# Kernel tuning notes

Hardware: AMD Instinct MI355X
Metric: run time of the kernel (lower is better)

The kernel has to match this reference:

```python
import jax, jax.numpy as jnp
import numpy as np

HID = 1024
H = 8        # num_attention_heads
KV = 2       # num_key_value_heads
HD = HID // H  # head_dim = 128
G = H // KV    # kv groups = 4
EPS = 1e-6


def setup_inputs() -> dict:
    key = jax.random.key(0)
    ks = jax.random.split(key, 12)
    B, S = 4, 2048
    s = 0.02
    inp = {
        "hidden_states": jax.random.normal(ks[0], (B, S, HID), jnp.float32),
        "rope": jax.random.normal(ks[1], (1, 1, S, 2 * HD), jnp.float32),
        # q_proj outputs 2*H*HD (query + elementwise gate)
        "Wq": jax.random.normal(ks[2], (HID, 2 * H * HD), jnp.float32) * s,
        "bq": jnp.zeros((2 * H * HD,), jnp.float32),
        "Wk": jax.random.normal(ks[3], (HID, KV * HD), jnp.float32) * s,
        "bk": jnp.zeros((KV * HD,), jnp.float32),
        "Wv": jax.random.normal(ks[4], (HID, KV * HD), jnp.float32) * s,
        "bv": jnp.zeros((KV * HD,), jnp.float32),
        "Wo": jax.random.normal(ks[5], (H * HD, HID), jnp.float32) * s,
        "bo": jnp.zeros((HID,), jnp.float32),
        "q_norm_w": jnp.ones((HD,), jnp.float32),
        "k_norm_w": jnp.ones((HD,), jnp.float32),
    }
    return inp


def _rmsnorm(x, w):
    var = jnp.mean(jnp.square(x), axis=-1, keepdims=True)
    return x * jax.lax.rsqrt(var + EPS) * w


def _rot(x):
    # interleaved rotation: [-x1, x0, -x3, x2, ...]
    x2 = x.reshape(x.shape[:-1] + (HD // 2, 2))
    r = jnp.stack([-x2[..., 1], x2[..., 0]], axis=-1)
    return r.reshape(x.shape)


def _apply_rope_cat(x, emb):
    # emb: [S, 2*HD] = cat(sin, cos); x: [B, h, S, HD]
    sin, cos = jnp.split(emb, 2, axis=-1)
    sin = sin[None, None]
    cos = cos[None, None]
    return x * cos + _rot(x) * sin


def reference(hidden_states, rope, Wq, bq, Wk, bk, Wv, bv, Wo, bo, q_norm_w, k_norm_w):
    B, S, _ = hidden_states.shape
    qg = hidden_states @ Wq + bq                     # [B,S,2*H*HD]
    qg = qg.reshape(B, S, KV, -1)                    # [B,S,KV, 2*G*HD]
    q, gate = jnp.split(qg, [HD * G], axis=-1)       # [B,S,KV,G*HD], [B,S,KV,G*HD]
    gate = gate.reshape(B, S, H, HD)                 # [B,S,H,HD]
    q = q.reshape(B, S, H, HD).transpose(0, 2, 1, 3) # [B,H,S,HD]
    k = (hidden_states @ Wk + bk).reshape(B, S, KV, HD).transpose(0, 2, 1, 3)
    v = (hidden_states @ Wv + bv).reshape(B, S, KV, HD).transpose(0, 2, 1, 3)

    q = _rmsnorm(q, q_norm_w)
    k = _rmsnorm(k, k_norm_w)

    emb = rope[0, 0, :S]                             # [S, 2*HD]
    q = _apply_rope_cat(q, emb)
    k = _apply_rope_cat(k, emb)

    # GQA: repeat kv heads to match query heads
    k = jnp.repeat(k, G, axis=1)                     # [B,H,S,HD]
    v = jnp.repeat(v, G, axis=1)

    scale = 1.0 / jnp.sqrt(jnp.asarray(HD, q.dtype))
    scores = jnp.einsum("bhqd,bhkd->bhqk", q, k) * scale
    attn = jax.nn.softmax(scores, axis=-1)
    out = jnp.einsum("bhqk,bhkd->bhqd", attn, v)     # [B,H,S,HD]

    out = out.transpose(0, 2, 1, 3)                  # [B,S,H,HD]
    out = out * jax.nn.sigmoid(gate)
    out = out.reshape(B, S, H * HD)
    return out @ Wo + bo
```

## Files before the change

### kernel.cpp

```cpp
#include <hip/hip_runtime.h>
#include <math.h>

#define SCALE_ 0.08838834764831845f
#define PSHIFT 8.0f
#define LOG2E_ 1.4426950408889634f
#define PSH2_  11.541560327111707f

typedef __attribute__((ext_vector_type(8))) short short8;
typedef __attribute__((ext_vector_type(4))) float floatx4;
typedef __attribute__((ext_vector_type(4))) _Float16 half4;
typedef __attribute__((ext_vector_type(8))) _Float16 half8;

__device__ inline short f2bf(float x) {
    union { float f; unsigned u; } v; v.f = x;
    unsigned r = v.u + 0x7fff + ((v.u >> 16) & 1);
    return (short)(r >> 16);
}
__device__ inline float bf2f(short h) {
    union { float f; unsigned u; } v; v.u = ((unsigned)(unsigned short)h) << 16;
    return v.f;
}

__global__ __launch_bounds__(256) void prep_fused(
    const float* __restrict__ X, short* __restrict__ Xb,
    const float* __restrict__ bq, const float* __restrict__ bk2,
    const float* __restrict__ bv2, float* __restrict__ bcat,
    const float* __restrict__ Wq, const float* __restrict__ Wk,
    const float* __restrict__ Wv, const float* __restrict__ Wo,
    short* __restrict__ Wt, short* __restrict__ Wot)
{
    __shared__ float T[32][33];
    const int bid = blockIdx.x;
    const int t = threadIdx.x;
    if (bid < 8192) {
        const int gid = bid * 256 + t;
        if (gid < 2097152) {
            const float4 v = ((const float4*)X)[gid];
            short4 o;
            o.x = f2bf(v.x); o.y = f2bf(v.y); o.z = f2bf(v.z); o.w = f2bf(v.w);
            ((short4*)Xb)[gid] = o;
        }
        if (gid < 2560)
            bcat[gid] = (gid < 2048) ? bq[gid]
                      : (gid < 2304) ? bk2[gid - 2048] : bv2[gid - 2304];
        return;
    }
    const int t2 = bid - 8192;
    const int k0 = (t2 & 31) * 32;
    const int ny = t2 >> 5;
    const float* src; int ldn, ncol0, nrow0; short* dst;
    if (ny < 80) {
        const int n0 = ny * 32;
        if (n0 < 2048)      { src = Wq; ldn = 2048; ncol0 = n0; }
        else if (n0 < 2304) { src = Wk; ldn = 256;  ncol0 = n0 - 2048; }
        else                { src = Wv; ldn = 256;  ncol0 = n0 - 2304; }
        dst = Wt; nrow0 = n0;
    } else {
        const int n0 = (ny - 80) * 32;
        src = Wo; ldn = 1024; ncol0 = n0; dst = Wot; nrow0 = n0;
    }
    {
        const int r = t >> 3, c4 = (t & 7) * 4;
        const float4 v = *(const float4*)&src[(size_t)(k0 + r) * ldn + ncol0 + c4];
        T[r][c4 + 0] = v.x; T[r][c4 + 1] = v.y; T[r][c4 + 2] = v.z; T[r][c4 + 3] = v.w;
    }
    __syncthreads();
    {
        const int nr = t >> 3, kc4 = (t & 7) * 4;
        short4 o;
        o.x = f2bf(T[kc4 + 0][nr]);
        o.y = f2bf(T[kc4 + 1][nr]);
        o.z = f2bf(T[kc4 + 2][nr]);
        o.w = f2bf(T[kc4 + 3][nr]);
        *(short4*)&dst[(size_t)(nrow0 + nr) * 1024 + k0 + kc4] = o;
    }
}

__global__ __launch_bounds__(256) void qkv_mfma(
    const short* __restrict__ Ag, const short* __restrict__ Bg,
    const float* __restrict__ bcat,
    short* __restrict__ qb, short* __restrict__ kb,
    short* __restrict__ vb, short* __restrict__ gateb)
{
    __shared__ short As[128 * 64];
    __shared__ short Bs[128 * 64];
    const int tid = threadIdx.x;
    const int wave = tid >> 6, lane = tid & 63;
    const int quad = lane >> 4, l16 = lane & 15;
    const int wm = wave & 1, wn = wave >> 1;
    const int lin = blockIdx.x;
    const int xcd = lin & 7;
    const int idx = lin >> 3;
    const int rr_ = idx / 20;
    const int m0 = (xcd * 8 + rr_) * 128;
    const int n0 = (idx - rr_ * 20) * 128;

    floatx4 acc[4][4] = {};

    for (int k0 = 0; k0 < 1024; k0 += 64) {
        __syncthreads();
        #pragma unroll
        for (int c = 0; c < 4; ++c) {
            const int blk = (c * 4 + wave) * 64 + lane;
            const int row = blk >> 3, p = blk & 7;
            const int col = (p ^ (row & 7)) << 3;
            __builtin_amdgcn_global_load_lds(
                (const __attribute__((address_space(1))) unsigned int*)(Ag + (size_t)(m0 + row) * 1024 + k0 + col),
                (__attribute__((address_space(3))) unsigned int*)&As[(c * 4 + wave) * 512],
                16, 0, 0);
            __builtin_amdgcn_global_load_lds(
                (const __attribute__((address_space(1))) unsigned int*)(Bg + (size_t)(n0 + row) * 1024 + k0 + col),
                (__attribute__((address_space(3))) unsigned int*)&Bs[(c * 4 + wave) * 512],
                16, 0, 0);
        }
        __syncthreads();
        #pragma unroll
        for (int ks = 0; ks < 2; ++ks) {
            short8 af[4], bfr[4];
            #pragma unroll
            for (int mt = 0; mt < 4; ++mt) {
                const int row = wm * 64 + mt * 16 + l16;
                const int p = (ks * 4 + quad) ^ (row & 7);
                af[mt] = *(const short8*)&As[row * 64 + p * 8];
            }
            #pragma unroll
            for (int nt = 0; nt < 4; ++nt) {
                const int row = wn * 64 + nt * 16 + l16;
                const int p = (ks * 4 + quad) ^ (row & 7);
                bfr[nt] = *(const short8*)&Bs[row * 64 + p * 8];
            }
            #pragma unroll
            for (int mt = 0; mt < 4; ++mt)
                #pragma unroll
                for (int nt = 0; nt < 4; ++nt)
                    acc[mt][nt] = __builtin_amdgcn_mfma_f32_16x16x32_bf16(af[mt], bfr[nt], acc[mt][nt], 0, 0, 0);
        }
    }

    #pragma unroll
    for (int nt = 0; nt < 4; ++nt) {
        const int n = n0 + wn * 64 + nt * 16 + l16;
        const float bias = bcat[n];
        #pragma unroll
        for (int mt = 0; mt < 4; ++mt) {
            #pragma unroll
            for (int r = 0; r < 4; ++r) {
                const int m = m0 + wm * 64 + mt * 16 + quad * 4 + r;
                const int b = m >> 11, s = m & 2047;
                const short o = f2bf(acc[mt][nt][r] + bias);
                if (n < 2048) {
                    const int kv = n >> 10, rr = n & 1023;
                    if (rr < 512) {
                        const int h = kv * 4 + (rr >> 7), d = rr & 127;
                        qb[(((size_t)(b * 8 + h)) * 2048 + s) * 128 + d] = o;
                    } else {
                        const int r2 = rr - 512;
                        const int h = kv * 4 + (r2 >> 7), d = r2 & 127;
                        gateb[(size_t)m * 1024 + h * 128 + d] = o;
                    }
                } else if (n < 2304) {
                    const int c = n - 2048;
                    kb[(((size_t)(b * 2 + (c >> 7))) * 2048 + s) * 128 + (c & 127)] = o;
                } else {
                    const int c = n - 2304;
                    vb[(((size_t)(b * 2 + (c >> 7))) * 2048 + s) * 128 + (c & 127)] = o;
                }
            }
        }
    }
}

__global__ __launch_bounds__(256) void norm_vtrans(
    short* __restrict__ qb, short* __restrict__ kb,
    const float* __restrict__ rope,
    const float* __restrict__ qw, const float* __restrict__ kw,
    const short* __restrict__ vb, _Float16* __restrict__ vt)
{
    __shared__ float T[32][33];
    const int bid = blockIdx.x;
    const int t = threadIdx.x;
    if (bid < 20480) {
        const int row = bid * 4 + (t >> 6);
        short* base; const float* w; int s; float scl;
        if (row < 65536) { base = qb + (size_t)row * 128; s = row & 2047; w = qw; scl = SCALE_; }
        else { const int r2 = row - 65536; base = kb + (size_t)r2 * 128; s = r2 & 2047; w = kw; scl = 1.0f; }
        const int lane = t & 63;
        const short2 xv = *(const short2*)&base[lane * 2];
        const float x0 = bf2f(xv.x), x1 = bf2f(xv.y);
        float ssq = x0 * x0 + x1 * x1;
        #pragma unroll
        for (int off = 1; off < 64; off <<= 1) ssq += __shfl_xor(ssq, off);
        const float inv = rsqrtf(ssq * (1.0f / 128.0f) + 1e-6f);
        const float a = x0 * inv * w[lane * 2];
        const float b = x1 * inv * w[lane * 2 + 1];
        const float* er = rope + (size_t)s * 256;
        const float sin0 = er[lane * 2], sin1 = er[lane * 2 + 1];
        const float cos0 = er[128 + lane * 2], cos1 = er[128 + lane * 2 + 1];
        short2 o;
        o.x = f2bf((a * cos0 - b * sin0) * scl);
        o.y = f2bf((b * cos1 + a * sin1) * scl);
        *(short2*)&base[lane * 2] = o;
        return;
    }
    const int t2 = bid - 20480;
    const int s0 = (t2 & 63) * 32, d0 = ((t2 >> 6) & 3) * 32, bk = t2 >> 8;
    const short* src = vb + ((size_t)bk * 2048 + s0) * 128 + d0;
    {
        const int sr = t >> 3, c4 = (t & 7) * 4;
        const short4 xv = *(const short4*)&src[sr * 128 + c4];
        T[sr][c4 + 0] = bf2f(xv.x);
        T[sr][c4 + 1] = bf2f(xv.y);
        T[sr][c4 + 2] = bf2f(xv.z);
        T[sr][c4 + 3] = bf2f(xv.w);
    }
    __syncthreads();
    {
        const int dr = t >> 3, sc4 = (t & 7) * 4;
        const int cs = sc4 >> 2;
        const int nc = (cs < 4) ? (cs << 1) : (((cs - 4) << 1) | 1);
        half4 o;
        o[0] = (_Float16)T[sc4 + 0][dr];
        o[1] = (_Float16)T[sc4 + 1][dr];
        o[2] = (_Float16)T[sc4 + 2][dr];
        o[3] = (_Float16)T[sc4 + 3][dr];
        *(half4*)&vt[((size_t)bk * 128 + d0 + dr) * 2048 + s0 + nc * 4] = o;
    }
}

__global__ __launch_bounds__(256, 2) void attn_mfma(
    const short* __restrict__ qb, const short* __restrict__ kb,
    const _Float16* __restrict__ vt, const short* __restrict__ gateb,
    short* __restrict__ xo)
{
    __shared__ short    Ks[2][64 * 128];
    __shared__ _Float16 VTs[2][128 * 64];

    const int tid = threadIdx.x;
    const int wave = tid >> 6, lane = tid & 63;
    const int quad = lane >> 4, l16 = lane & 15;
    const int lin = blockIdx.x;
    const int idx = lin >> 3;
    const int bh = (lin & 7) * 4 + (idx >> 4);
    const int b = bh >> 3, h = bh & 7, kv = h >> 2;
    const int q0 = (idx & 15) * 128;

    short8 qf[4][2];
    #pragma unroll
    for (int u = 0; u < 2; ++u) {
        const short* qbase = qb + (((size_t)(b * 8 + h)) * 2048 + q0 + wave * 32 + u * 16 + l16) * 128;
        #pragma unroll
        for (int ks = 0; ks < 4; ++ks)
            qf[ks][u] = *(const short8*)&qbase[ks * 32 + quad * 8];
    }

    const short*    kbase  = kb + (size_t)(b * 2 + kv) * 2048 * 128;
    const _Float16* vtbase = vt + (size_t)(b * 2 + kv) * 128 * 2048;

    int koff[4], voff[4];
    #pragma unroll
    for (int c = 0; c < 4; ++c) {
        const int sidx = (c * 4 + wave) * 64 + lane;
        { const int r = sidx >> 4, p = sidx & 15;
          koff[c] = r * 128 + ((p ^ (r & 7)) << 3); }
        { const int r = sidx >> 3, p = sidx & 7;
          voff[c] = r * 2048 + ((p ^ (r & 7)) << 3); }
    }

    floatx4 O[8][2] = {};
    float lsum[2] = {0.0f, 0.0f};

    #pragma unroll
    for (int c = 0; c < 4; ++c) {
        __builtin_amdgcn_global_load_lds(
            (const __attribute__((address_space(1))) unsigned int*)(kbase + koff[c]),
            (__attribute__((address_space(3))) unsigned int*)&Ks[0][(c * 4 + wave) * 512],
            16, 0, 0);
        __builtin_amdgcn_global_load_lds(
            (const __attribute__((address_space(1))) unsigned int*)(vtbase + voff[c]),
            (__attribute__((address_space(3))) unsigned int*)&VTs[0][(c * 4 + wave) * 512],
            16, 0, 0);
    }

    for (int kt = 0; kt < 32; ++kt) {
        const int cur = kt & 1;
        __syncthreads();

        if (kt + 1 < 32) {
            const short*    kg = kbase  + (size_t)(kt + 1) * 8192;
            const _Float16* vg = vtbase + (kt + 1) * 64;
            #pragma unroll
            for (int c = 0; c < 4; ++c) {
                __builtin_amdgcn_global_load_lds(
                    (const __attribute__((address_space(1))) unsigned int*)(kg + koff[c]),
                    (__attribute__((address_space(3))) unsigned int*)&Ks[cur ^ 1][(c * 4 + wave) * 512],
                    16, 0, 0);
                __builtin_amdgcn_global_load_lds(
                    (const __attribute__((address_space(1))) unsigned int*)(vg + voff[c]),
                    (__attribute__((address_space(3))) unsigned int*)&VTs[cur ^ 1][(c * 4 + wave) * 512],
                    16, 0, 0);
            }
        }

        #pragma unroll
        for (int t = 0; t < 2; ++t) {
            floatx4 ST[2][2];
            __builtin_amdgcn_s_setprio(1);
            #pragma unroll
            for (int j = 0; j < 2; ++j) {
                ST[j][0] = (floatx4){0.f, 0.f, 0.f, 0.f};
                ST[j][1] = (floatx4){0.f, 0.f, 0.f, 0.f};
                const int krow = (2 * t + j) * 16 + l16;
                #pragma unroll
                for (int ks = 0; ks < 4; ++ks) {
                    const short8 af = *(const short8*)&Ks[cur][krow * 128 + (((ks * 4 + quad) ^ (l16 & 7)) << 3)];
                    ST[j][0] = __builtin_amdgcn_mfma_f32_16x16x32_bf16(af, qf[ks][0], ST[j][0], 0, 0, 0);
                    ST[j][1] = __builtin_amdgcn_mfma_f32_16x16x32_bf16(af, qf[ks][1], ST[j][1], 0, 0, 0);
                }
            }
            __builtin_amdgcn_s_setprio(0);

            half8 pf[2];
            #pragma unroll
            for (int u = 0; u < 2; ++u) {
                #pragma unroll
                for (int r = 0; r < 4; ++r) {
                    const float plo = exp2f(fmaf(ST[0][u][r], LOG2E_, -PSH2_));
                    const float phi = exp2f(fmaf(ST[1][u][r], LOG2E_, -PSH2_));
                    lsum[u] += plo + phi;
                    pf[u][r]     = (_Float16)plo;
                    pf[u][4 + r] = (_Float16)phi;
                }
            }

            __builtin_amdgcn_s_setprio(1);
            #pragma unroll
            for (int dt = 0; dt < 8; ++dt) {
                const half8 va = *(const half8*)&VTs[cur][(dt * 16 + l16) * 64 + (((4 * t + quad) ^ (l16 & 7)) << 3)];
                O[dt][0] = __builtin_amdgcn_mfma_f32_16x16x32_f16(va, pf[0], O[dt][0], 0, 0, 0);
                O[dt][1] = __builtin_amdgcn_mfma_f32_16x16x32_f16(va, pf[1], O[dt][1], 0, 0, 0);
            }
            __builtin_amdgcn_s_setprio(0);
        }
    }

    #pragma unroll
    for (int u = 0; u < 2; ++u) {
        float ps = lsum[u];
        ps += __shfl_xor(ps, 16);
        ps += __shfl_xor(ps, 32);
        const float invl = 1.0f / ps;
        const int s = q0 + wave * 32 + u * 16 + l16;
        const size_t base = ((size_t)b * 2048 + s) * 1024 + h * 128;
        #pragma unroll
        for (int dt = 0; dt < 8; ++dt) {
            const int d0 = dt * 16 + quad * 4;
            const short4 g4 = *(const short4*)&gateb[base + d0];
            short4 o4;
            o4.x = f2bf(O[dt][u][0] * invl * (1.0f / (1.0f + __expf(-bf2f(g4.x)))));
            o4.y = f2bf(O[dt][u][1] * invl * (1.0f / (1.0f + __expf(-bf2f(g4.y)))));
            o4.z = f2bf(O[dt][u][2] * invl * (1.0f / (1.0f + __expf(-bf2f(g4.z)))));
            o4.w = f2bf(O[dt][u][3] * invl * (1.0f / (1.0f + __expf(-bf2f(g4.w)))));
            *(short4*)&xo[base + d0] = o4;
        }
    }
}

__global__ __launch_bounds__(256) void out_mfma(
    const short* __restrict__ Ag, const short* __restrict__ Bg,
    const float* __restrict__ bo, float* __restrict__ Y)
{
    __shared__ short As[128 * 64];
    __shared__ short Bs[128 * 64];
    const int tid = threadIdx.x;
    const int wave = tid >> 6, lane = tid & 63;
    const int quad = lane >> 4, l16 = lane & 15;
    const int wm = wave & 1, wn = wave >> 1;
    const int lin = blockIdx.x;
    const int xcd = lin & 7;
    const int idx = lin >> 3;
    const int m0 = (xcd * 8 + (idx >> 3)) * 128;
    const int n0 = (idx & 7) * 128;

    floatx4 acc[4][4] = {};

    for (int k0 = 0; k0 < 1024; k0 += 64) {
        __syncthreads();
        #pragma unroll
        for (int c = 0; c < 4; ++c) {
            const int blk = (c * 4 + wave) * 64 + lane;
            const int row = blk >> 3, p = blk & 7;
            const int col = (p ^ (row & 7)) << 3;
            __builtin_amdgcn_global_load_lds(
                (const __attribute__((address_space(1))) unsigned int*)(Ag + (size_t)(m0 + row) * 1024 + k0 + col),
                (__attribute__((address_space(3))) unsigned int*)&As[(c * 4 + wave) * 512],
                16, 0, 0);
            __builtin_amdgcn_global_load_lds(
                (const __attribute__((address_space(1))) unsigned int*)(Bg + (size_t)(n0 + row) * 1024 + k0 + col),
                (__attribute__((address_space(3))) unsigned int*)&Bs[(c * 4 + wave) * 512],
                16, 0, 0);
        }
        __syncthreads();
        #pragma unroll
        for (int ks = 0; ks < 2; ++ks) {
            short8 af[4], bfr[4];
            #pragma unroll
            for (int mt = 0; mt < 4; ++mt) {
                const int row = wm * 64 + mt * 16 + l16;
                const int p = (ks * 4 + quad) ^ (row & 7);
                af[mt] = *(const short8*)&As[row * 64 + p * 8];
            }
            #pragma unroll
            for (int nt = 0; nt < 4; ++nt) {
                const int row = wn * 64 + nt * 16 + l16;
                const int p = (ks * 4 + quad) ^ (row & 7);
                bfr[nt] = *(const short8*)&Bs[row * 64 + p * 8];
            }
            #pragma unroll
            for (int mt = 0; mt < 4; ++mt)
                #pragma unroll
                for (int nt = 0; nt < 4; ++nt)
                    acc[mt][nt] = __builtin_amdgcn_mfma_f32_16x16x32_bf16(af[mt], bfr[nt], acc[mt][nt], 0, 0, 0);
        }
    }

    #pragma unroll
    for (int nt = 0; nt < 4; ++nt) {
        const int n = n0 + wn * 64 + nt * 16 + l16;
        const float bias = bo[n];
        #pragma unroll
        for (int mt = 0; mt < 4; ++mt) {
            #pragma unroll
            for (int r = 0; r < 4; ++r) {
                const int m = m0 + wm * 64 + mt * 16 + quad * 4 + r;
                Y[(size_t)m * 1024 + n] = acc[mt][nt][r] + bias;
            }
        }
    }
}

extern "C" void kernel_launch(void* const* d_in, const int* in_sizes, int n_in,
                              void* d_out, int out_size, void* d_ws, size_t ws_size,
                              hipStream_t stream) {
    (void)in_sizes; (void)n_in; (void)out_size; (void)ws_size;
    const float* hs   = (const float*)d_in[0];
    const float* rope = (const float*)d_in[1];
    const float* Wq   = (const float*)d_in[2];
    const float* bq   = (const float*)d_in[3];
    const float* Wk   = (const float*)d_in[4];
    const float* bk   = (const float*)d_in[5];
    const float* Wv   = (const float*)d_in[6];
    const float* bv   = (const float*)d_in[7];
    const float* Wo   = (const float*)d_in[8];
    const float* bo   = (const float*)d_in[9];
    const float* qw   = (const float*)d_in[10];
    const float* kw   = (const float*)d_in[11];
    float* out = (float*)d_out;

    short* qb    = (short*)d_ws;
    short* kbuf  = qb    + (size_t)8388608;
    short* vb    = kbuf  + (size_t)2097152;
    _Float16* vt = (_Float16*)(vb + (size_t)2097152);
    short* gateb = (short*)(vt + (size_t)2097152);
    short* xb    = gateb + (size_t)8388608;
    short* wt    = xb    + (size_t)8388608;
    short* wot   = wt    + (size_t)2621440;
    float* bcat  = (float*)(wot + (size_t)1048576);

    prep_fused<<<dim3(11776), 256, 0, stream>>>(hs, xb, bq, bk, bv, bcat,
                                                Wq, Wk, Wv, Wo, wt, wot);
    qkv_mfma<<<dim3(1280), 256, 0, stream>>>(xb, wt, bcat, qb, kbuf, vb, gateb);
    norm_vtrans<<<dim3(22528), 256, 0, stream>>>(qb, kbuf, rope, qw, kw, vb, vt);
    attn_mfma<<<dim3(512), 256, 0, stream>>>(qb, kbuf, vt, gateb, xb);
    out_mfma<<<dim3(512), 256, 0, stream>>>(xb, wot, bo, out);
}
```

Before: 308.1 us.

## Split attention KV tiles across two wave groups with LDS combine

The attention kernel moves from 256 to 512 threads per block. Two wave groups each process half of every 64-key tile for the same query rows, then the second group's partial O accumulators and row sums are written to LDS and merged by the first group before the gated store. The aim is more resident waves to hide latency and half the serial MFMA chain per wave. In exchange it adds a reduction through LDS and drops the s_setprio hints. The __launch_bounds__(512,4) request may also force very tight register limits, which risks spilling the O accumulators.

Measured after the change: 387.7 us. 1.26x slower.

```diff
diff --git a/kernel.cpp b/kernel.cpp
--- a/kernel.cpp
+++ b/kernel.cpp
@@ -227,17 +227,21 @@
     }
 }
 
-__global__ __launch_bounds__(256, 2) void attn_mfma(
+__global__ __launch_bounds__(512, 4) void attn_mfma(
     const short* __restrict__ qb, const short* __restrict__ kb,
     const _Float16* __restrict__ vt, const short* __restrict__ gateb,
     short* __restrict__ xo)
 {
-    __shared__ short    Ks[2][64 * 128];
-    __shared__ _Float16 VTs[2][128 * 64];
+    __shared__ __align__(16) char smem[67584];
+    short*    KsB  = (short*)smem;
+    _Float16* VTsB = (_Float16*)(smem + 32768);
+    floatx4*  comb = (floatx4*)smem;
+    float*    Lred = (float*)(smem + 65536);
 
     const int tid = threadIdx.x;
     const int wave = tid >> 6, lane = tid & 63;
     const int quad = lane >> 4, l16 = lane & 15;
+    const int qg = wave & 3, kh = wave >> 2;
     const int lin = blockIdx.x;
     const int idx = lin >> 3;
     const int bh = (lin & 7) * 4 + (idx >> 4);
@@ -247,7 +251,7 @@
     short8 qf[4][2];
     #pragma unroll
     for (int u = 0; u < 2; ++u) {
-        const short* qbase = qb + (((size_t)(b * 8 + h)) * 2048 + q0 + wave * 32 + u * 16 + l16) * 128;
+        const short* qbase = qb + (((size_t)(b * 8 + h)) * 2048 + q0 + qg * 32 + u * 16 + l16) * 128;
         #pragma unroll
         for (int ks = 0; ks < 4; ++ks)
             qf[ks][u] = *(const short8*)&qbase[ks * 32 + quad * 8];
@@ -256,10 +260,10 @@
     const short*    kbase  = kb + (size_t)(b * 2 + kv) * 2048 * 128;
     const _Float16* vtbase = vt + (size_t)(b * 2 + kv) * 128 * 2048;
 
-    int koff[4], voff[4];
+    int koff[2], voff[2];
     #pragma unroll
-    for (int c = 0; c < 4; ++c) {
-        const int sidx = (c * 4 + wave) * 64 + lane;
+    for (int c = 0; c < 2; ++c) {
+        const int sidx = (c * 8 + wave) * 64 + lane;
         { const int r = sidx >> 4, p = sidx & 15;
           koff[c] = r * 128 + ((p ^ (r & 7)) << 3); }
         { const int r = sidx >> 3, p = sidx & 7;
@@ -270,14 +274,14 @@
     float lsum[2] = {0.0f, 0.0f};
 
     #pragma unroll
-    for (int c = 0; c < 4; ++c) {
+    for (int c = 0; c < 2; ++c) {
         __builtin_amdgcn_global_load_lds(
             (const __attribute__((address_space(1))) unsigned int*)(kbase + koff[c]),
-            (__attribute__((address_space(3))) unsigned int*)&Ks[0][(c * 4 + wave) * 512],
+            (__attribute__((address_space(3))) unsigned int*)&KsB[(c * 8 + wave) * 512],
             16, 0, 0);
         __builtin_amdgcn_global_load_lds(
             (const __attribute__((address_space(1))) unsigned int*)(vtbase + voff[c]),
-            (__attribute__((address_space(3))) unsigned int*)&VTs[0][(c * 4 + wave) * 512],
+            (__attribute__((address_space(3))) unsigned int*)&VTsB[(c * 8 + wave) * 512],
             16, 0, 0);
     }
 
@@ -289,78 +293,85 @@
             const short*    kg = kbase  + (size_t)(kt + 1) * 8192;
             const _Float16* vg = vtbase + (kt + 1) * 64;
             #pragma unroll
-            for (int c = 0; c < 4; ++c) {
+            for (int c = 0; c < 2; ++c) {
                 __builtin_amdgcn_global_load_lds(
                     (const __attribute__((address_space(1))) unsigned int*)(kg + koff[c]),
-                    (__attribute__((address_space(3))) unsigned int*)&Ks[cur ^ 1][(c * 4 + wave) * 512],
+                    (__attribute__((address_space(3))) unsigned int*)&KsB[(cur ^ 1) * 8192 + (c * 8 + wave) * 512],
                     16, 0, 0);
                 __builtin_amdgcn_global_load_lds(
                     (const __attribute__((address_space(1))) unsigned int*)(vg + voff[c]),
-                    (__attribute__((address_space(3))) unsigned int*)&VTs[cur ^ 1][(c * 4 + wave) * 512],
+                    (__attribute__((address_space(3))) unsigned int*)&VTsB[(cur ^ 1) * 8192 + (c * 8 + wave) * 512],
                     16, 0, 0);
             }
         }
 
-        #pragma unroll
-        for (int t = 0; t < 2; ++t) {
-            floatx4 ST[2][2];
-            __builtin_amdgcn_s_setprio(1);
-            #pragma unroll
-            for (int j = 0; j < 2; ++j) {
-                ST[j][0] = (floatx4){0.f, 0.f, 0.f, 0.f};
-                ST[j][1] = (floatx4){0.f, 0.f, 0.f, 0.f};
-                const int krow = (2 * t + j) * 16 + l16;
-                #pragma unroll
-                for (int ks = 0; ks < 4; ++ks) {
-                    const short8 af = *(const short8*)&Ks[cur][krow * 128 + (((ks * 4 + quad) ^ (l16 & 7)) << 3)];
-                    ST[j][0] = __builtin_amdgcn_mfma_f32_16x16x32_bf16(af, qf[ks][0], ST[j][0], 0, 0, 0);
-                    ST[j][1] = __builtin_amdgcn_mfma_f32_16x16x32_bf16(af, qf[ks][1], ST[j][1], 0, 0, 0);
-                }
-            }
-            __builtin_amdgcn_s_setprio(0);
-
-            half8 pf[2];
-            #pragma unroll
-            for (int u = 0; u < 2; ++u) {
-                #pragma unroll
-                for (int r = 0; r < 4; ++r) {
-                    const float plo = exp2f(fmaf(ST[0][u][r], LOG2E_, -PSH2_));
-                    const float phi = exp2f(fmaf(ST[1][u][r], LOG2E_, -PSH2_));
-                    lsum[u] += plo + phi;
-                    pf[u][r]     = (_Float16)plo;
-                    pf[u][4 + r] = (_Float16)phi;
-                }
-            }
-
-            __builtin_amdgcn_s_setprio(1);
+        floatx4 ST[2][2];
+        #pragma unroll
+        for (int jr = 0; jr < 2; ++jr) {
+            ST[jr][0] = (floatx4){0.f, 0.f, 0.f, 0.f};
+            ST[jr][1] = (floatx4){0.f, 0.f, 0.f, 0.f};
+            const int krow = kh * 32 + jr * 16 + l16;
+            #pragma unroll
+            for (int ks = 0; ks < 4; ++ks) {
+                const short8 af = *(const short8*)&KsB[cur * 8192 + krow * 128 + (((ks * 4 + quad) ^ (l16 & 7)) << 3)];
+                ST[jr][0] = __builtin_amdgcn_mfma_f32_16x16x32_bf16(af, qf[ks][0], ST[jr][0], 0, 0, 0);
+                ST[jr][1] = __builtin_amdgcn_mfma_f32_16x16x32_bf16(af, qf[ks][1], ST[jr][1], 0, 0, 0);
+            }
+        }
+
+        half8 pf[2];
+        #pragma unroll
+        for (int u = 0; u < 2; ++u) {
+            #pragma unroll
+            for (int r = 0; r < 4; ++r) {
+                const float plo = exp2f(fmaf(ST[0][u][r], LOG2E_, -PSH2_));
+                const float phi = exp2f(fmaf(ST[1][u][r], LOG2E_, -PSH2_));
+                lsum[u] += plo + phi;
+                pf[u][r]     = (_Float16)plo;
+                pf[u][4 + r] = (_Float16)phi;
+            }
+        }
+
+        #pragma unroll
+        for (int dt = 0; dt < 8; ++dt) {
+            const half8 va = *(const half8*)&VTsB[cur * 8192 + (dt * 16 + l16) * 64 + (((4 * kh + quad) ^ (l16 & 7)) << 3)];
+            O[dt][0] = __builtin_amdgcn_mfma_f32_16x16x32_f16(va, pf[0], O[dt][0], 0, 0, 0);
+            O[dt][1] = __builtin_amdgcn_mfma_f32_16x16x32_f16(va, pf[1], O[dt][1], 0, 0, 0);
+        }
+    }
+
+    __syncthreads();
+    if (kh == 1) {
+        #pragma unroll
+        for (int u = 0; u < 2; ++u) {
+            Lred[(qg * 2 + u) * 64 + lane] = lsum[u];
+            #pragma unroll
+            for (int dt = 0; dt < 8; ++dt)
+                comb[((qg * 2 + u) * 8 + dt) * 64 + lane] = O[dt][u];
+        }
+    }
+    __syncthreads();
+    if (kh == 0) {
+        #pragma unroll
+        for (int u = 0; u < 2; ++u) {
+            float ps = lsum[u] + Lred[(qg * 2 + u) * 64 + lane];
+            ps += __shfl_xor(ps, 16);
+            ps += __shfl_xor(ps, 32);
+            const float invl = 1.0f / ps;
+            const int s = q0 + qg * 32 + u * 16 + l16;
+            const size_t base = ((size_t)b * 2048 + s) * 1024 + h * 128;
             #pragma unroll
             for (int dt = 0; dt < 8; ++dt) {
-                const half8 va = *(const half8*)&VTs[cur][(dt * 16 + l16) * 64 + (((4 * t + quad) ^ (l16 & 7)) << 3)];
-                O[dt][0] = __builtin_amdgcn_mfma_f32_16x16x32_f16(va, pf[0], O[dt][0], 0, 0, 0);
-                O[dt][1] = __builtin_amdgcn_mfma_f32_16x16x32_f16(va, pf[1], O[dt][1], 0, 0, 0);
-            }
-            __builtin_amdgcn_s_setprio(0);
-        }
-    }
-
-    #pragma unroll
-    for (int u = 0; u < 2; ++u) {
-        float ps = lsum[u];
-        ps += __shfl_xor(ps, 16);
-        ps += __shfl_xor(ps, 32);
-        const float invl = 1.0f / ps;
-        const int s = q0 + wave * 32 + u * 16 + l16;
-        const size_t base = ((size_t)b * 2048 + s) * 1024 + h * 128;
-        #pragma unroll
-        for (int dt = 0; dt < 8; ++dt) {
-            const int d0 = dt * 16 + quad * 4;
-            const short4 g4 = *(const short4*)&gateb[base + d0];
-            short4 o4;
-            o4.x = f2bf(O[dt][u][0] * invl * (1.0f / (1.0f + __expf(-bf2f(g4.x)))));
-            o4.y = f2bf(O[dt][u][1] * invl * (1.0f / (1.0f + __expf(-bf2f(g4.y)))));
-            o4.z = f2bf(O[dt][u][2] * invl * (1.0f / (1.0f + __expf(-bf2f(g4.z)))));
-            o4.w = f2bf(O[dt][u][3] * invl * (1.0f / (1.0f + __expf(-bf2f(g4.w)))));
-            *(short4*)&xo[base + d0] = o4;
+                const floatx4 oc = O[dt][u] + comb[((qg * 2 + u) * 8 + dt) * 64 + lane];
+                const int d0 = dt * 16 + quad * 4;
+                const short4 g4 = *(const short4*)&gateb[base + d0];
+                short4 o4;
+                o4.x = f2bf(oc[0] * invl * (1.0f / (1.0f + __expf(-bf2f(g4.x)))));
+                o4.y = f2bf(oc[1] * invl * (1.0f / (1.0f + __expf(-bf2f(g4.y)))));
+                o4.z = f2bf(oc[2] * invl * (1.0f / (1.0f + __expf(-bf2f(g4.z)))));
+                o4.w = f2bf(oc[3] * invl * (1.0f / (1.0f + __expf(-bf2f(g4.w)))));
+                *(short4*)&xo[base + d0] = o4;
+            }
         }
     }
 }
@@ -470,6 +481,6 @@
                                                 Wq, Wk, Wv, Wo, wt, wot);
     qkv_mfma<<<dim3(1280), 256, 0, stream>>>(xb, wt, bcat, qb, kbuf, vb, gateb);
     norm_vtrans<<<dim3(22528), 256, 0, stream>>>(qb, kbuf, rope, qw, kw, vb, vt);
-    attn_mfma<<<dim3(512), 256, 0, stream>>>(qb, kbuf, vt, gateb, xb);
+    attn_mfma<<<dim3(512), 512, 0, stream>>>(qb, kbuf, vt, gateb, xb);
     out_mfma<<<dim3(512), 256, 0, stream>>>(xb, wot, bo, out);
 }
```
